# Kernel tuning notes

Hardware: AMD Instinct MI355X
Metric: run time of the kernel (lower is better)

The kernel has to match this reference:

```python
import jax, jax.numpy as jnp
import numpy as np

B, N, CIN, H, UNITS = 8, 2048, 256, 256, 256


def setup_inputs() -> dict:
    key = jax.random.key(0)
    ks = jax.random.split(key, 7)
    s = 1.0 / np.sqrt(CIN)
    return {
        "x": jax.random.normal(ks[0], (B, N, CIN), dtype=jnp.float32),
        "Wq": jax.random.normal(ks[1], (CIN, H), dtype=jnp.float32) * s,
        "bq": jax.random.normal(ks[2], (H,), dtype=jnp.float32) * 0.01,
        "Wk": jax.random.normal(ks[3], (CIN, H), dtype=jnp.float32) * s,
        "bk": jax.random.normal(ks[4], (H,), dtype=jnp.float32) * 0.01,
        "Wm": jax.random.normal(ks[5], (H, UNITS), dtype=jnp.float32) * (1.0 / np.sqrt(H)),
        "bm": jax.random.normal(ks[6], (UNITS,), dtype=jnp.float32) * 0.01,
    }


def reference(x, Wq, bq, Wk, bk, Wm, bm):
    # Dense projections with fused relu (as in the Keras module)
    q = jax.nn.relu(x @ Wq + bq)          # (B,N,H)
    k = jax.nn.relu(x @ Wk + bk)          # (B,N,H)
    v = q                                 # NOTE: source uses fc_query for value (fc_value unused)
    # Unscaled key @ query^T, softmax over last axis
    kq = jax.nn.softmax(jnp.einsum('bnh,bmh->bnm', k, q), axis=-1)  # (B,N,N)
    # value^T @ kq, then Permute((2,1)): att[b,m,h] = sum_n v[b,n,h] * kq[b,n,m]
    att = jnp.einsum('bnh,bnm->bmh', v, kq)                          # (B,N,H)
    return jax.nn.relu(att @ Wm + bm)                                # (B,N,UNITS)
```

## Files before the change

### kernel.cpp

```cpp
#include <hip/hip_runtime.h>
#include <hip/hip_bf16.h>
#include <math.h>

#define BB   8
#define NN   2048
#define CC   256
#define MTOT (BB * NN)

typedef __bf16 bf16_t;
typedef bf16_t    bf16x8 __attribute__((ext_vector_type(8)));
typedef _Float16  halfx8 __attribute__((ext_vector_type(8)));
typedef float     floatx4 __attribute__((ext_vector_type(4)));

#define LOG2E 1.44269504088896f

__device__ __forceinline__ void gl_lds16(const bf16_t* g, bf16_t* l) {
    __builtin_amdgcn_global_load_lds(
        (const __attribute__((address_space(1))) unsigned int*)g,
        (__attribute__((address_space(3))) unsigned int*)l, 16, 0, 0);
}

template<int OMODE, bool BIASRELU, bool DO_STATS>
__global__ __launch_bounds__(256, 3)
void gemm_nt(const bf16_t* __restrict__ A, const bf16_t* __restrict__ B,
             void* __restrict__ C, const float* __restrict__ bias,
             int lda, int ldb, int ldc, int swz,
             long strideA, long strideB, long strideC,
             float* __restrict__ pm, float* __restrict__ pl)
{
    int b, m0, n0, myi;
    if (swz) {
        b = blockIdx.x & 7;
        const int r = blockIdx.x >> 3;
        n0  = (r % swz) * 128;
        myi = r / swz;
        m0  = myi * 128;
    } else {
        b   = blockIdx.z;
        m0  = blockIdx.y * 128;
        n0  = blockIdx.x * 128;
        myi = blockIdx.y;
    }
    A += (long)b * strideA;
    B += (long)b * strideB;

    __shared__ bf16_t As[128 * 64];
    __shared__ bf16_t Bs[128 * 64];
    __shared__ float  smx[4][4][16];
    __shared__ float  ssm[4][4][16];

    const int tid  = threadIdx.x;
    const int wid  = tid >> 6, lane = tid & 63;
    const int wm   = (wid >> 1) * 64, wn = (wid & 1) * 64;
    const int fr   = lane & 15;
    const int u16  = lane >> 4;
    const int fsw  = fr & 7;

    floatx4 acc[4][4] = {};

    for (int k0 = 0; k0 < 256; k0 += 64) {
#pragma unroll
        for (int r = 0; r < 4; ++r) {
            const int lin = tid + r * 256;
            const int rw  = lin >> 3, kc = lin & 7;
            const int kcs = kc ^ (rw & 7);
            gl_lds16(A + (long)(m0 + rw) * lda + k0 + kcs * 8, As + lin * 8);
            gl_lds16(B + (long)(n0 + rw) * ldb + k0 + kcs * 8, Bs + lin * 8);
        }
        __syncthreads();
        bf16x8 af[4][2], bf[4][2];
#pragma unroll
        for (int f = 0; f < 4; ++f)
#pragma unroll
            for (int j = 0; j < 2; ++j) {
                const int chunk = (j * 4 + u16) ^ fsw;
                af[f][j] = *(const bf16x8*)(As + (wm + f * 16 + fr) * 64 + chunk * 8);
                bf[f][j] = *(const bf16x8*)(Bs + (wn + f * 16 + fr) * 64 + chunk * 8);
            }
#pragma unroll
        for (int j = 0; j < 2; ++j)
#pragma unroll
            for (int f = 0; f < 4; ++f)
#pragma unroll
                for (int g = 0; g < 4; ++g)
                    acc[f][g] = __builtin_amdgcn_mfma_f32_16x16x32_bf16(af[f][j], bf[g][j], acc[f][g], 0, 0, 0);
        __syncthreads();
    }

    const int rbase = u16 * 4;
#pragma unroll
    for (int g = 0; g < 4; ++g) {
        const int n = n0 + wn + g * 16 + fr;
        const float bv = BIASRELU ? bias[n] : 0.0f;
#pragma unroll
        for (int f = 0; f < 4; ++f) {
#pragma unroll
            for (int r = 0; r < 4; ++r) {
                const int m = m0 + wm + f * 16 + rbase + r;
                float v = acc[f][g][r] + bv;
                if (BIASRELU) v = v > 0.0f ? v : 0.0f;
                if (OMODE == 0)
                    ((float*)C)[(long)b * strideC + (long)m * ldc + n] = v;
                else if (OMODE == 1)
                    ((bf16_t*)C)[(long)b * strideC + (long)m * ldc + n] = (bf16_t)v;
                else
                    ((_Float16*)C)[(long)b * strideC + (long)m * ldc + n] = (_Float16)v;
            }
        }
    }

    if (DO_STATS) {
        float lmax[4], lsum[4];
#pragma unroll
        for (int g = 0; g < 4; ++g) {
            float m = -1e30f;
#pragma unroll
            for (int f = 0; f < 4; ++f)
#pragma unroll
                for (int r = 0; r < 4; ++r) m = fmaxf(m, acc[f][g][r]);
            m = fmaxf(m, __shfl_xor(m, 16));
            m = fmaxf(m, __shfl_xor(m, 32));
            float s = 0.0f;
#pragma unroll
            for (int f = 0; f < 4; ++f)
#pragma unroll
                for (int r = 0; r < 4; ++r) s += __expf(acc[f][g][r] - m);
            s += __shfl_xor(s, 16);
            s += __shfl_xor(s, 32);
            lmax[g] = m; lsum[g] = s;
        }
        if (lane < 16) {
#pragma unroll
            for (int g = 0; g < 4; ++g) {
                smx[wid][g][lane] = lmax[g];
                ssm[wid][g][lane] = lsum[g];
            }
        }
        __syncthreads();
        if (tid < 128) {
            const int pair = tid >> 6;
            const int idx  = tid & 63;
            const int g = idx >> 4, f2 = idx & 15;
            const float m0v = smx[pair][g][f2], m1v = smx[pair + 2][g][f2];
            const float M = fmaxf(m0v, m1v);
            const float L = ssm[pair][g][f2] * __expf(m0v - M) +
                            ssm[pair + 2][g][f2] * __expf(m1v - M);
            const int n = n0 + pair * 64 + g * 16 + f2;
            const long o = ((long)b * 16 + myi) * NN + n;
            pm[o] = M;
            pl[o] = L;
        }
    }
}

__global__ __launch_bounds__(256)
void stats_combine(const float* __restrict__ pm, const float* __restrict__ pl,
                   float* __restrict__ c2)
{
    const int i = blockIdx.x * 256 + threadIdx.x;
    const int b = i >> 11, n = i & 2047;
    float M = -1e30f, L = 0.0f;
#pragma unroll
    for (int t = 0; t < 16; ++t) {
        const long o = ((long)b * 16 + t) * NN + n;
        const float m = pm[o], l = pl[o];
        const float nm = fmaxf(M, m);
        L = L * __expf(M - nm) + l * __expf(m - nm);
        M = nm;
    }
    c2[i] = (M + logf(L)) * LOG2E;
}

#define APAD 68
__global__ __launch_bounds__(256, 4)
void att_out(const _Float16* __restrict__ St, const bf16_t* __restrict__ qmT,
             const float* __restrict__ c2, const float* __restrict__ bm,
             float* __restrict__ out)
{
    const int bid = blockIdx.x;
    const int b   = bid & 7;
    const int r   = bid >> 3;
    const int m0  = (r >> 1) * 32;
    const int u0  = (r & 1) * 128;
    const _Float16* S  = St  + (long)b * NN * NN;
    const bf16_t*   Q  = qmT + (long)b * 256 * NN;
    const float*    C2 = c2  + b * NN;
    float*          O  = out + (long)b * NN * 256;

    __shared__ bf16_t As[32 * APAD];
    __shared__ bf16_t Bs[128 * 64];

    const int tid  = threadIdx.x;
    const int wid  = tid >> 6, lane = tid & 63;
    const int wm2  = (wid >> 1) * 16;
    const int wu   = (wid & 1) * 64;
    const int fr   = lane & 15;
    const int u16  = lane >> 4;
    const int kb   = u16 * 8;
    const int fsw  = fr & 7;
    const int arow = tid >> 3;
    const int aseg = tid & 7;

    const _Float16* Srow = S + (long)(m0 + arow) * NN + aseg * 8;

    floatx4 acc[4] = {};

    for (int n0 = 0; n0 < NN; n0 += 64) {
#pragma unroll
        for (int r2 = 0; r2 < 4; ++r2) {
            const int lin = tid + r2 * 256;
            const int rw  = lin >> 3, kc = lin & 7;
            const int kcs = kc ^ (rw & 7);
            gl_lds16(Q + (long)(u0 + rw) * NN + n0 + kcs * 8, Bs + lin * 8);
        }
        const halfx8 hv = *(const halfx8*)(Srow + n0);
        const float4 ca = *(const float4*)(C2 + n0 + aseg * 8);
        const float4 cb = *(const float4*)(C2 + n0 + aseg * 8 + 4);
        bf16x8 p;
        p[0] = (bf16_t)exp2f(fmaf((float)hv[0], LOG2E, -ca.x));
        p[1] = (bf16_t)exp2f(fmaf((float)hv[1], LOG2E, -ca.y));
        p[2] = (bf16_t)exp2f(fmaf((float)hv[2], LOG2E, -ca.z));
        p[3] = (bf16_t)exp2f(fmaf((float)hv[3], LOG2E, -ca.w));
        p[4] = (bf16_t)exp2f(fmaf((float)hv[4], LOG2E, -cb.x));
        p[5] = (bf16_t)exp2f(fmaf((float)hv[5], LOG2E, -cb.y));
        p[6] = (bf16_t)exp2f(fmaf((float)hv[6], LOG2E, -cb.z));
        p[7] = (bf16_t)exp2f(fmaf((float)hv[7], LOG2E, -cb.w));
        *(bf16x8*)(As + arow * APAD + aseg * 8) = p;
        __syncthreads();

        bf16x8 af[2], bg[4][2];
#pragma unroll
        for (int j = 0; j < 2; ++j)
            af[j] = *(const bf16x8*)(As + (wm2 + fr) * APAD + j * 32 + kb);
#pragma unroll
        for (int g = 0; g < 4; ++g)
#pragma unroll
            for (int j = 0; j < 2; ++j) {
                const int chunk = (j * 4 + u16) ^ fsw;
                bg[g][j] = *(const bf16x8*)(Bs + (wu + g * 16 + fr) * 64 + chunk * 8);
            }
#pragma unroll
        for (int j = 0; j < 2; ++j)
#pragma unroll
            for (int g = 0; g < 4; ++g)
                acc[g] = __builtin_amdgcn_mfma_f32_16x16x32_bf16(af[j], bg[g][j], acc[g], 0, 0, 0);
        __syncthreads();
    }

    const int rbase = u16 * 4;
#pragma unroll
    for (int g = 0; g < 4; ++g) {
        const int u = u0 + wu + g * 16 + fr;
        const float bvv = bm[u];
#pragma unroll
        for (int r2 = 0; r2 < 4; ++r2) {
            const int m = m0 + wm2 + rbase + r2;
            const float v = acc[g][r2] + bvv;
            O[(long)m * 256 + u] = v > 0.0f ? v : 0.0f;
        }
    }
}

__global__ __launch_bounds__(256)
void cvt_bf16(const float* __restrict__ x, bf16_t* __restrict__ y)
{
    const long i = ((long)blockIdx.x * 256 + threadIdx.x) * 8;
    const float4 a = *(const float4*)(x + i);
    const float4 b = *(const float4*)(x + i + 4);
    bf16x8 o;
    o[0] = (bf16_t)a.x; o[1] = (bf16_t)a.y; o[2] = (bf16_t)a.z; o[3] = (bf16_t)a.w;
    o[4] = (bf16_t)b.x; o[5] = (bf16_t)b.y; o[6] = (bf16_t)b.z; o[7] = (bf16_t)b.w;
    *(bf16x8*)(y + i) = o;
}

__global__ __launch_bounds__(256)
void prep_w(const float* __restrict__ Wq, const float* __restrict__ Wk,
            const float* __restrict__ Wm, const float* __restrict__ bq,
            const float* __restrict__ bk, bf16_t* __restrict__ WqkT,
            bf16_t* __restrict__ WmT, float* __restrict__ bqk)
{
    const int z = blockIdx.z;
    const float* W = (z == 0) ? Wq : (z == 1) ? Wk : Wm;
    bf16_t* Wt = (z == 0) ? WqkT : (z == 1) ? (WqkT + 256 * 256) : WmT;
    __shared__ float t[32][33];
    const int n0 = blockIdx.x * 32, k0 = blockIdx.y * 32;
    const int tx = threadIdx.x & 31, ty = threadIdx.x >> 5;
    for (int i = ty; i < 32; i += 8) t[i][tx] = W[(k0 + i) * 256 + n0 + tx];
    __syncthreads();
    for (int i = ty; i < 32; i += 8) Wt[(n0 + i) * 256 + k0 + tx] = (bf16_t)t[tx][i];
    if (z == 0 && blockIdx.x == 0 && blockIdx.y == 0) {
        bqk[threadIdx.x]       = bq[threadIdx.x];
        bqk[256 + threadIdx.x] = bk[threadIdx.x];
    }
}

extern "C" void kernel_launch(void* const* d_in, const int* in_sizes, int n_in,
                              void* d_out, int out_size, void* d_ws, size_t ws_size,
                              hipStream_t stream)
{
    (void)in_sizes; (void)n_in; (void)out_size; (void)ws_size;
    const float* x  = (const float*)d_in[0];
    const float* Wq = (const float*)d_in[1];
    const float* bq = (const float*)d_in[2];
    const float* Wk = (const float*)d_in[3];
    const float* bk = (const float*)d_in[4];
    const float* Wm = (const float*)d_in[5];
    const float* bm = (const float*)d_in[6];
    float* out = (float*)d_out;

    char* w = (char*)d_ws;
    _Float16* St   = (_Float16*)w;                  w += (size_t)BB * NN * NN * 2;
    bf16_t* x_bf   = (bf16_t*)w;                    w += (size_t)MTOT * 256 * 2;
    bf16_t* qk     = (bf16_t*)w;                    w += (size_t)MTOT * 512 * 2;
    bf16_t* qmT    = (bf16_t*)w;                    w += (size_t)MTOT * 256 * 2;
    bf16_t* WqkT   = (bf16_t*)w;                    w += 512 * 256 * 2;
    bf16_t* WmT    = (bf16_t*)w;                    w += 256 * 256 * 2;
    float*  bqk    = (float*)w;                     w += 512 * 4;
    float*  pm     = (float*)w;                     w += (size_t)BB * 16 * NN * 4;
    float*  pl     = (float*)w;                     w += (size_t)BB * 16 * NN * 4;
    float*  c2b    = (float*)w;

    cvt_bf16<<<dim3(MTOT * 256 / (256 * 8)), 256, 0, stream>>>(x, x_bf);
    prep_w<<<dim3(8, 8, 3), 256, 0, stream>>>(Wq, Wk, Wm, bq, bk, WqkT, WmT, bqk);

    gemm_nt<1, true, false><<<dim3(4, 128, 1), 256, 0, stream>>>(
        x_bf, WqkT, qk, bqk, 256, 256, 512, 0, 0, 0, 0, nullptr, nullptr);

    gemm_nt<1, false, false><<<dim3(256, 1, 1), 256, 0, stream>>>(
        WmT, qk, qmT, nullptr, 256, 512, NN, 16,
        0, (long)NN * 512, (long)256 * NN, nullptr, nullptr);

    gemm_nt<2, false, true><<<dim3(2048, 1, 1), 256, 0, stream>>>(
        qk, qk + 256, St, nullptr, 512, 512, NN, 16,
        (long)NN * 512, (long)NN * 512, (long)NN * NN, pm, pl);

    stats_combine<<<dim3(MTOT / 256), 256, 0, stream>>>(pm, pl, c2b);

    att_out<<<dim3(1024, 1, 1), 256, 0, stream>>>(St, qmT, c2b, bm, out);
}
```

Measured before the change: 172.9 us.

## Use dedicated 256x128-tile score GEMM with 512 threads and fewer partial stats

Splits the score-matrix GEMM out of the generic kernel into a dedicated kernel. The new kernel uses 256x128 tiles with 8 waves per block, which halves the grid and the number of per-row-block softmax partials (16 to 8). Each B tile is now reused across twice as many rows, and the stats-combine pass reads fewer partials. In exchange it uses more LDS per block, and the lower wave occupancy limit may reduce latency hiding.

```diff
diff --git a/kernel.cpp b/kernel.cpp
--- a/kernel.cpp
+++ b/kernel.cpp
@@ -20,34 +20,29 @@
         (__attribute__((address_space(3))) unsigned int*)l, 16, 0, 0);
 }
 
-template<int OMODE, bool BIASRELU, bool DO_STATS>
+template<int OMODE, bool BIASRELU>
 __global__ __launch_bounds__(256, 3)
 void gemm_nt(const bf16_t* __restrict__ A, const bf16_t* __restrict__ B,
              void* __restrict__ C, const float* __restrict__ bias,
              int lda, int ldb, int ldc, int swz,
-             long strideA, long strideB, long strideC,
-             float* __restrict__ pm, float* __restrict__ pl)
-{
-    int b, m0, n0, myi;
-    if (swz) {
+             long strideA, long strideB, long strideC)
+{
+    int b, m0, n0;
+    if (swz > 0) {
         b = blockIdx.x & 7;
         const int r = blockIdx.x >> 3;
-        n0  = (r % swz) * 128;
-        myi = r / swz;
-        m0  = myi * 128;
+        n0 = (r % swz) * 128;
+        m0 = (r / swz) * 128;
     } else {
-        b   = blockIdx.z;
-        m0  = blockIdx.y * 128;
-        n0  = blockIdx.x * 128;
-        myi = blockIdx.y;
+        b  = blockIdx.z;
+        m0 = blockIdx.y * 128;
+        n0 = blockIdx.x * 128;
     }
     A += (long)b * strideA;
     B += (long)b * strideB;
 
     __shared__ bf16_t As[128 * 64];
     __shared__ bf16_t Bs[128 * 64];
-    __shared__ float  smx[4][4][16];
-    __shared__ float  ssm[4][4][16];
 
     const int tid  = threadIdx.x;
     const int wid  = tid >> 6, lane = tid & 63;
@@ -108,48 +103,130 @@
             }
         }
     }
-
-    if (DO_STATS) {
-        float lmax[4], lsum[4];
+}
+
+__global__ __launch_bounds__(512, 2)
+void gemm_st(const bf16_t* __restrict__ A, const bf16_t* __restrict__ B,
+             _Float16* __restrict__ C,
+             int lda, int ldb, int ldc,
+             long strideA, long strideB, long strideC,
+             float* __restrict__ pm, float* __restrict__ pl)
+{
+    const int b   = blockIdx.x & 7;
+    const int r   = blockIdx.x >> 3;
+    const int n0  = (r & 15) * 128;
+    const int myi = r >> 4;
+    const int m0  = myi * 256;
+    A += (long)b * strideA;
+    B += (long)b * strideB;
+
+    __shared__ bf16_t As[256 * 64];
+    __shared__ bf16_t Bs[128 * 64];
+    __shared__ float  smx[8][4][16];
+    __shared__ float  ssm[8][4][16];
+
+    const int tid  = threadIdx.x;
+    const int wid  = tid >> 6, lane = tid & 63;
+    const int wm   = (wid >> 1) * 64;
+    const int wn   = (wid & 1) * 64;
+    const int fr   = lane & 15;
+    const int u16  = lane >> 4;
+    const int fsw  = fr & 7;
+
+    floatx4 acc[4][4] = {};
+
+    for (int k0 = 0; k0 < 256; k0 += 64) {
+#pragma unroll
+        for (int rr = 0; rr < 4; ++rr) {
+            const int lin = tid + rr * 512;
+            const int rw  = lin >> 3, kc = lin & 7;
+            const int kcs = kc ^ (rw & 7);
+            gl_lds16(A + (long)(m0 + rw) * lda + k0 + kcs * 8, As + lin * 8);
+        }
+#pragma unroll
+        for (int rr = 0; rr < 2; ++rr) {
+            const int lin = tid + rr * 512;
+            const int rw  = lin >> 3, kc = lin & 7;
+            const int kcs = kc ^ (rw & 7);
+            gl_lds16(B + (long)(n0 + rw) * ldb + k0 + kcs * 8, Bs + lin * 8);
+        }
+        __syncthreads();
+        bf16x8 af[4][2], bf[4][2];
+#pragma unroll
+        for (int f = 0; f < 4; ++f)
+#pragma unroll
+            for (int j = 0; j < 2; ++j) {
+                const int chunk = (j * 4 + u16) ^ fsw;
+                af[f][j] = *(const bf16x8*)(As + (wm + f * 16 + fr) * 64 + chunk * 8);
+                bf[f][j] = *(const bf16x8*)(Bs + (wn + f * 16 + fr) * 64 + chunk * 8);
+            }
+#pragma unroll
+        for (int j = 0; j < 2; ++j)
+#pragma unroll
+            for (int f = 0; f < 4; ++f)
+#pragma unroll
+                for (int g = 0; g < 4; ++g)
+                    acc[f][g] = __builtin_amdgcn_mfma_f32_16x16x32_bf16(af[f][j], bf[g][j], acc[f][g], 0, 0, 0);
+        __syncthreads();
+    }
+
+    const int rbase = u16 * 4;
+#pragma unroll
+    for (int g = 0; g < 4; ++g) {
+        const int n = n0 + wn + g * 16 + fr;
+#pragma unroll
+        for (int f = 0; f < 4; ++f)
+#pragma unroll
+            for (int rr = 0; rr < 4; ++rr) {
+                const int m = m0 + wm + f * 16 + rbase + rr;
+                C[(long)b * strideC + (long)m * ldc + n] = (_Float16)acc[f][g][rr];
+            }
+    }
+
+    float lmax[4], lsum[4];
+#pragma unroll
+    for (int g = 0; g < 4; ++g) {
+        float m = -1e30f;
+#pragma unroll
+        for (int f = 0; f < 4; ++f)
+#pragma unroll
+            for (int rr = 0; rr < 4; ++rr) m = fmaxf(m, acc[f][g][rr]);
+        m = fmaxf(m, __shfl_xor(m, 16));
+        m = fmaxf(m, __shfl_xor(m, 32));
+        float s = 0.0f;
+#pragma unroll
+        for (int f = 0; f < 4; ++f)
+#pragma unroll
+            for (int rr = 0; rr < 4; ++rr) s += __expf(acc[f][g][rr] - m);
+        s += __shfl_xor(s, 16);
+        s += __shfl_xor(s, 32);
+        lmax[g] = m; lsum[g] = s;
+    }
+    if (lane < 16) {
 #pragma unroll
         for (int g = 0; g < 4; ++g) {
-            float m = -1e30f;
-#pragma unroll
-            for (int f = 0; f < 4; ++f)
-#pragma unroll
-                for (int r = 0; r < 4; ++r) m = fmaxf(m, acc[f][g][r]);
-            m = fmaxf(m, __shfl_xor(m, 16));
-            m = fmaxf(m, __shfl_xor(m, 32));
-            float s = 0.0f;
-#pragma unroll
-            for (int f = 0; f < 4; ++f)
-#pragma unroll
-                for (int r = 0; r < 4; ++r) s += __expf(acc[f][g][r] - m);
-            s += __shfl_xor(s, 16);
-            s += __shfl_xor(s, 32);
-            lmax[g] = m; lsum[g] = s;
-        }
-        if (lane < 16) {
-#pragma unroll
-            for (int g = 0; g < 4; ++g) {
-                smx[wid][g][lane] = lmax[g];
-                ssm[wid][g][lane] = lsum[g];
-            }
-        }
-        __syncthreads();
-        if (tid < 128) {
-            const int pair = tid >> 6;
-            const int idx  = tid & 63;
-            const int g = idx >> 4, f2 = idx & 15;
-            const float m0v = smx[pair][g][f2], m1v = smx[pair + 2][g][f2];
-            const float M = fmaxf(m0v, m1v);
-            const float L = ssm[pair][g][f2] * __expf(m0v - M) +
-                            ssm[pair + 2][g][f2] * __expf(m1v - M);
-            const int n = n0 + pair * 64 + g * 16 + f2;
-            const long o = ((long)b * 16 + myi) * NN + n;
-            pm[o] = M;
-            pl[o] = L;
-        }
+            smx[wid][g][lane] = lmax[g];
+            ssm[wid][g][lane] = lsum[g];
+        }
+    }
+    __syncthreads();
+    if (tid < 128) {
+        const int nh = tid >> 6;
+        const int idx = tid & 63;
+        const int g = idx >> 4, f2 = idx & 15;
+        float M = smx[nh][g][f2], L = ssm[nh][g][f2];
+#pragma unroll
+        for (int mw = 1; mw < 4; ++mw) {
+            const float m2 = smx[2 * mw + nh][g][f2];
+            const float l2 = ssm[2 * mw + nh][g][f2];
+            const float nm = fmaxf(M, m2);
+            L = L * __expf(M - nm) + l2 * __expf(m2 - nm);
+            M = nm;
+        }
+        const int n = n0 + nh * 64 + g * 16 + f2;
+        const long o = ((long)b * 8 + myi) * NN + n;
+        pm[o] = M;
+        pl[o] = L;
     }
 }
 
@@ -161,8 +238,8 @@
     const int b = i >> 11, n = i & 2047;
     float M = -1e30f, L = 0.0f;
 #pragma unroll
-    for (int t = 0; t < 16; ++t) {
-        const long o = ((long)b * 16 + t) * NN + n;
+    for (int t = 0; t < 8; ++t) {
+        const long o = ((long)b * 8 + t) * NN + n;
         const float m = pm[o], l = pl[o];
         const float nm = fmaxf(M, m);
         L = L * __expf(M - nm) + l * __expf(m - nm);
@@ -316,22 +393,22 @@
     bf16_t* WqkT   = (bf16_t*)w;                    w += 512 * 256 * 2;
     bf16_t* WmT    = (bf16_t*)w;                    w += 256 * 256 * 2;
     float*  bqk    = (float*)w;                     w += 512 * 4;
-    float*  pm     = (float*)w;                     w += (size_t)BB * 16 * NN * 4;
-    float*  pl     = (float*)w;                     w += (size_t)BB * 16 * NN * 4;
+    float*  pm     = (float*)w;                     w += (size_t)BB * 8 * NN * 4;
+    float*  pl     = (float*)w;                     w += (size_t)BB * 8 * NN * 4;
     float*  c2b    = (float*)w;
 
     cvt_bf16<<<dim3(MTOT * 256 / (256 * 8)), 256, 0, stream>>>(x, x_bf);
     prep_w<<<dim3(8, 8, 3), 256, 0, stream>>>(Wq, Wk, Wm, bq, bk, WqkT, WmT, bqk);
 
-    gemm_nt<1, true, false><<<dim3(4, 128, 1), 256, 0, stream>>>(
-        x_bf, WqkT, qk, bqk, 256, 256, 512, 0, 0, 0, 0, nullptr, nullptr);
-
-    gemm_nt<1, false, false><<<dim3(256, 1, 1), 256, 0, stream>>>(
+    gemm_nt<1, true><<<dim3(4, 128, 1), 256, 0, stream>>>(
+        x_bf, WqkT, qk, bqk, 256, 256, 512, 0, 0, 0, 0);
+
+    gemm_nt<1, false><<<dim3(256, 1, 1), 256, 0, stream>>>(
         WmT, qk, qmT, nullptr, 256, 512, NN, 16,
-        0, (long)NN * 512, (long)256 * NN, nullptr, nullptr);
-
-    gemm_nt<2, false, true><<<dim3(2048, 1, 1), 256, 0, stream>>>(
-        qk, qk + 256, St, nullptr, 512, 512, NN, 16,
+        0, (long)NN * 512, (long)256 * NN);
+
+    gemm_st<<<dim3(1024, 1, 1), 512, 0, stream>>>(
+        qk, qk + 256, St, 512, 512, NN,
         (long)NN * 512, (long)NN * 512, (long)NN * NN, pm, pl);
 
     stats_combine<<<dim3(MTOT / 256), 256, 0, stream>>>(pm, pl, c2b);
```

Result: slower. 181.7 us (+5.1%).
